# Optimization experiments

Hardware: AMD Instinct MI355X
Metric: run time of the kernel (lower is better)

Reference implementation:

```python
import jax, jax.numpy as jnp
import numpy as np

N_NODES = 100000
N_EDGES = 3200000
NUM_FEATURES = 128


def gcn_conv(x, edge_index, W, b):
    """PyG-style GCNConv: symmetric normalization with self-loops.
    x: [N, F_in], edge_index: [2, E] (row=src, col=dst), W: [F_in, F_out], b: [F_out].
    """
    n = x.shape[0]
    h = x @ W  # [N, F_out]
    # add self loops
    loop = jnp.arange(n, dtype=edge_index.dtype)
    row = jnp.concatenate([edge_index[0], loop])  # src
    col = jnp.concatenate([edge_index[1], loop])  # dst
    # degree of destination nodes (with self loops), edge weight = 1
    ones = jnp.ones(row.shape[0], dtype=h.dtype)
    deg = jax.ops.segment_sum(ones, col, num_segments=n)  # [N]
    dinv = jnp.where(deg > 0, jax.lax.rsqrt(deg), 0.0)
    norm = dinv[row] * dinv[col]  # [E+N]
    msg = h[row] * norm[:, None]  # gather + scale, [E+N, F_out]
    out = jax.ops.segment_sum(msg, col, num_segments=n)  # scatter-add
    return out + b


def setup_inputs() -> dict:
    key = jax.random.key(0)
    k1, k2, k3, k4 = jax.random.split(key, 4)
    x = jax.random.normal(k1, (N_NODES, NUM_FEATURES), dtype=jnp.float32)
    edge_index = jax.random.randint(k2, (2, N_EDGES), 0, N_NODES, dtype=jnp.int64)
    W1 = jax.random.normal(k3, (NUM_FEATURES, 16), dtype=jnp.float32) * (1.0 / np.sqrt(NUM_FEATURES))
    b1 = jnp.zeros((16,), dtype=jnp.float32)
    W2 = jax.random.normal(k4, (16, 2), dtype=jnp.float32) * (1.0 / np.sqrt(16.0))
    b2 = jnp.zeros((2,), dtype=jnp.float32)
    return {"x": x, "edge_index": edge_index, "W1": W1, "b1": b1, "W2": W2, "b2": b2}


def reference(x, edge_index, W1, b1, W2, b2):
    h = gcn_conv(x, edge_index, W1, b1)
    h = jax.nn.relu(h)
    out = gcn_conv(h, edge_index, W2, b2)
    return out
```

## Files before the change

kernel.cpp:

```cpp
#include <hip/hip_runtime.h>

#define N_FEAT 128
#define F1 16
#define F2 2
#define XPAD 132
#define NPB 512
#define NPB_SHIFT 9
#define BMAX 256
#define CHUNK 8192
#define HBLK 1024
#define K2 4

typedef int   ev_i4 __attribute__((ext_vector_type(4)));
typedef float ev_f4 __attribute__((ext_vector_type(4)));

__device__ __forceinline__ int4 nt_load_i4(const void* p) {
    ev_i4 v = __builtin_nontemporal_load((const ev_i4*)p);
    return make_int4(v.x, v.y, v.z, v.w);
}
__device__ __forceinline__ int nt_load_i(const int* p) {
    return __builtin_nontemporal_load(p);
}
__device__ __forceinline__ float4 nt_load_f4(const void* p) {
    ev_f4 v = __builtin_nontemporal_load((const ev_f4*)p);
    return make_float4(v.x, v.y, v.z, v.w);
}

__global__ __launch_bounds__(256) void hist_kernel(const int* __restrict__ col, int E,
        int* __restrict__ bcnt) {
    __shared__ int hist[BMAX];
    int t = threadIdx.x;
    hist[t] = 0;
    __syncthreads();
    int nq = (E + 3) >> 2;
    for (int q = blockIdx.x * 256 + t; q < nq; q += HBLK * 256) {
        int e0 = q * 4;
        if (e0 + 3 < E) {
            int4 c = nt_load_i4(col + e0);
            atomicAdd(&hist[c.x >> NPB_SHIFT], 1);
            atomicAdd(&hist[c.y >> NPB_SHIFT], 1);
            atomicAdd(&hist[c.z >> NPB_SHIFT], 1);
            atomicAdd(&hist[c.w >> NPB_SHIFT], 1);
        } else {
            for (int e = e0; e < E; ++e) atomicAdd(&hist[col[e] >> NPB_SHIFT], 1);
        }
    }
    __syncthreads();
    if (hist[t]) atomicAdd(&bcnt[t], hist[t]);
}

__global__ __launch_bounds__(256) void bscan_kernel(const int* __restrict__ bcnt,
        int* __restrict__ bstart, int* __restrict__ gcur, int E, int nbuck) {
    __shared__ int s[BMAX];
    int t = threadIdx.x;
    int v = (t < nbuck) ? bcnt[t] : 0;
    s[t] = v;
    __syncthreads();
    for (int off = 1; off < BMAX; off <<= 1) {
        int a = (t >= off) ? s[t - off] : 0;
        __syncthreads();
        s[t] += a;
        __syncthreads();
    }
    int excl = s[t] - v;
    if (t < nbuck) { bstart[t] = excl; gcur[t] = excl; }
    if (t == 0) bstart[nbuck] = E;
}

__global__ __launch_bounds__(256) void bin_kernel(const int* __restrict__ rowi,
        const int* __restrict__ coli, int* __restrict__ gcur,
        int* __restrict__ ebin, int E) {
    __shared__ int stage[CHUNK];
    __shared__ unsigned char sbkt[CHUNK];
    __shared__ int cnt[BMAX];
    __shared__ int pos[BMAX];
    __shared__ int runb[BMAX];
    int t = threadIdx.x;
    int base = blockIdx.x * CHUNK;
    int nval = E - base; if (nval > CHUNK) nval = CHUNK;
    cnt[t] = 0;
    __syncthreads();

    int cbuf[32];
#pragma unroll
    for (int j = 0; j < 8; ++j) {
        int idx = base + ((j << 8) + t) * 4;
        if (idx + 3 < E) {
            int4 c4 = nt_load_i4(coli + idx);
            cbuf[j * 4 + 0] = c4.x; cbuf[j * 4 + 1] = c4.y;
            cbuf[j * 4 + 2] = c4.z; cbuf[j * 4 + 3] = c4.w;
        } else {
#pragma unroll
            for (int u = 0; u < 4; ++u) {
                int i2 = idx + u;
                cbuf[j * 4 + u] = (i2 < E) ? coli[i2] : -1;
            }
        }
    }
#pragma unroll
    for (int k = 0; k < 32; ++k)
        if (cbuf[k] >= 0) atomicAdd(&cnt[cbuf[k] >> NPB_SHIFT], 1);
    __syncthreads();

    pos[t] = cnt[t];
    __syncthreads();
    for (int off = 1; off < BMAX; off <<= 1) {
        int a = (t >= off) ? pos[t - off] : 0;
        __syncthreads();
        pos[t] += a;
        __syncthreads();
    }
    int myc = cnt[t];
    int excl = pos[t] - myc;
    if (myc > 0) {
        int g = atomicAdd(&gcur[t], myc);
        runb[t] = g - excl;
    }
    __syncthreads();
    cnt[t] = excl;
    __syncthreads();

#pragma unroll
    for (int j = 0; j < 8; ++j) {
        int idx = base + ((j << 8) + t) * 4;
        int rr[4];
        if (idx + 3 < E) {
            int4 r4 = nt_load_i4(rowi + idx);
            rr[0] = r4.x; rr[1] = r4.y; rr[2] = r4.z; rr[3] = r4.w;
        } else {
#pragma unroll
            for (int u = 0; u < 4; ++u) {
                int i2 = idx + u;
                rr[u] = (i2 < E) ? rowi[i2] : 0;
            }
        }
#pragma unroll
        for (int u = 0; u < 4; ++u) {
            int c = cbuf[j * 4 + u];
            if (c >= 0) {
                int b = c >> NPB_SHIFT;
                int lp = atomicAdd(&cnt[b], 1);
                stage[lp] = (rr[u] << NPB_SHIFT) | (c & (NPB - 1));
                sbkt[lp] = (unsigned char)b;
            }
        }
    }
    __syncthreads();
    for (int i = t; i < nval; i += 256)
        ebin[runb[sbkt[i]] + i] = stage[i];
}

__global__ __launch_bounds__(256) void degpart_kernel(const int* __restrict__ bstart,
        const int* __restrict__ ebin, int* __restrict__ degp) {
    __shared__ int cnt[NPB];
    int t = threadIdx.x;
    int bid = blockIdx.x;
    int b = bid / K2, slice = bid - b * K2;
    cnt[t] = 0; cnt[t + 256] = 0;
    __syncthreads();
    int s = bstart[b], e = bstart[b + 1];
    int per = (e - s + K2 - 1) / K2;
    int s0 = s + slice * per;
    int e0 = s0 + per; if (e0 > e) e0 = e;
    for (int i = s0 + t; i < e0; i += 1024) {
        int w[4];
#pragma unroll
        for (int u = 0; u < 4; ++u) {
            int idx = i + u * 256;
            w[u] = (idx < e0) ? nt_load_i(&ebin[idx]) : -1;
        }
#pragma unroll
        for (int u = 0; u < 4; ++u)
            if (w[u] >= 0) atomicAdd(&cnt[w[u] & (NPB - 1)], 1);
    }
    __syncthreads();
    int* dp = degp + (size_t)bid * NPB;
    dp[t] = cnt[t];
    dp[t + 256] = cnt[t + 256];
}

__global__ __launch_bounds__(256) void rowscan_kernel(const int* __restrict__ bstart,
        const int* __restrict__ degp, int* __restrict__ rstart,
        float* __restrict__ dinv, int N, int E) {
    __shared__ int sd[NPB];
    int b = blockIdx.x, t = threadIdx.x;
    int base = b << NPB_SHIFT;
    int d0 = 0, d1 = 0;
    for (int sl = 0; sl < K2; ++sl) {
        const int* dp = degp + (size_t)(b * K2 + sl) * NPB;
        d0 += dp[t]; d1 += dp[t + 256];
    }
    sd[t] = d0; sd[t + 256] = d1;
    __syncthreads();
    for (int off = 1; off < NPB; off <<= 1) {
        int a0 = (t >= off) ? sd[t - off] : 0;
        int a1 = (t + 256 >= off) ? sd[t + 256 - off] : 0;
        __syncthreads();
        sd[t] += a0; sd[t + 256] += a1;
        __syncthreads();
    }
    int bs = bstart[b];
    int g0 = base + t, g1 = base + t + 256;
    if (g0 < N) { rstart[g0] = bs + sd[t] - d0;        dinv[g0] = rsqrtf((float)(d0 + 1)); }
    if (g1 < N) { rstart[g1] = bs + sd[t + 256] - d1;  dinv[g1] = rsqrtf((float)(d1 + 1)); }
    if (b == 0 && t == 0) rstart[N] = E;
}

__global__ __launch_bounds__(256) void nodescat_kernel(const int* __restrict__ bstart,
        const int* __restrict__ rstart, const int* __restrict__ ebin,
        int* __restrict__ csr, int N) {
    __shared__ int cur[128];
    int t = threadIdx.x;
    int bid = blockIdx.x;
    int b = bid >> 2, q = bid & 3;
    int lo = q << 7;
    if (t < 128) {
        int g = (b << NPB_SHIFT) + lo + t;
        cur[t] = (g < N) ? rstart[g] : 0;
    }
    __syncthreads();
    int s = bstart[b], e = bstart[b + 1];
    for (int i = s + t; i < e; i += 1024) {
        int w[4];
#pragma unroll
        for (int u = 0; u < 4; ++u) {
            int idx = i + u * 256;
            w[u] = (idx < e) ? ebin[idx] : -1;
        }
#pragma unroll
        for (int u = 0; u < 4; ++u) {
            if (w[u] >= 0) {
                int n = (w[u] & (NPB - 1)) - lo;
                if ((unsigned)n < 128u) {
                    int p = atomicAdd(&cur[n], 1);
                    csr[p] = w[u] >> NPB_SHIFT;
                }
            }
        }
    }
}

__global__ __launch_bounds__(256) void gemm1_kernel(
    const float* __restrict__ x, const float* __restrict__ W1,
    const float* __restrict__ dinv, float* __restrict__ hs, int N) {
    __shared__ __align__(16) float wsT[F1][XPAD];
    __shared__ __align__(16) float xs[16][XPAD];
    int t = threadIdx.x;
    for (int i = t; i < N_FEAT * F1; i += 256) {
        int k = i >> 4, f = i & 15;
        wsT[f][k] = W1[i];
    }
    int row0 = blockIdx.x * 16;
    for (int i = t; i < 16 * (N_FEAT / 4); i += 256) {
        int r = i >> 5, k4 = i & 31;
        int row = row0 + r;
        float4 v = (row < N) ? nt_load_f4(x + (size_t)row * N_FEAT + k4 * 4)
                             : make_float4(0.f, 0.f, 0.f, 0.f);
        *(float4*)&xs[r][k4 * 4] = v;
    }
    __syncthreads();
    int rr = t >> 4, f = t & 15;
    int row = row0 + rr;
    if (row >= N) return;
    float acc = 0.f;
#pragma unroll
    for (int k4 = 0; k4 < 32; ++k4) {
        float4 xv = *(const float4*)&xs[rr][k4 * 4];
        float4 wv = *(const float4*)&wsT[f][k4 * 4];
        acc += xv.x * wv.x + xv.y * wv.y + xv.z * wv.z + xv.w * wv.w;
    }
    hs[(size_t)row * F1 + f] = acc * dinv[row];
}

__global__ __launch_bounds__(256) void agg1_kernel(const int* __restrict__ rstart,
        const int* __restrict__ csr, const float* __restrict__ hs,
        const float* __restrict__ dinv, const float* __restrict__ b1,
        const float* __restrict__ W2, float* __restrict__ hs2, int N) {
    int t = threadIdx.x;
    int g = blockIdx.x * 16 + (t >> 4);
    int f = t & 15;
    if (g >= N) return;
    int s = rstart[g], e = rstart[g + 1];
    float acc = hs[(size_t)g * F1 + f];
    int k = s;
    for (; k + 4 <= e; k += 4) {
        int s0 = nt_load_i(&csr[k]);
        int s1 = nt_load_i(&csr[k + 1]);
        int s2 = nt_load_i(&csr[k + 2]);
        int s3 = nt_load_i(&csr[k + 3]);
        float v0 = hs[(size_t)s0 * F1 + f];
        float v1 = hs[(size_t)s1 * F1 + f];
        float v2 = hs[(size_t)s2 * F1 + f];
        float v3 = hs[(size_t)s3 * F1 + f];
        acc += (v0 + v1) + (v2 + v3);
    }
    for (; k < e; ++k) acc += hs[(size_t)nt_load_i(&csr[k]) * F1 + f];
    float di = dinv[g];
    float o = fmaxf(di * acc + b1[f], 0.f);
    float h0 = o * W2[f * F2 + 0];
    float h1 = o * W2[f * F2 + 1];
#pragma unroll
    for (int off = 1; off < 16; off <<= 1) {
        h0 += __shfl_xor(h0, off);
        h1 += __shfl_xor(h1, off);
    }
    if (f == 0) *(float2*)&hs2[(size_t)g * 2] = make_float2(di * h0, di * h1);
}

__global__ __launch_bounds__(256) void agg2_kernel(const int* __restrict__ rstart,
        const int* __restrict__ csr, const float* __restrict__ hs2,
        const float* __restrict__ dinv, const float* __restrict__ b2,
        float* __restrict__ out, int N) {
    int t = threadIdx.x;
    int g = blockIdx.x * 64 + (t >> 2);
    int l = t & 3;
    if (g >= N) return;
    int j = l & 1, c = l >> 1;
    int s = rstart[g], e = rstart[g + 1];
    float acc = 0.f;
    int k = s + c;
    for (; k + 6 < e; k += 8) {
        int s0 = nt_load_i(&csr[k]);
        int s1 = nt_load_i(&csr[k + 2]);
        int s2 = nt_load_i(&csr[k + 4]);
        int s3 = nt_load_i(&csr[k + 6]);
        acc += hs2[(size_t)s0 * 2 + j] + hs2[(size_t)s1 * 2 + j]
             + hs2[(size_t)s2 * 2 + j] + hs2[(size_t)s3 * 2 + j];
    }
    for (; k < e; k += 2) acc += hs2[(size_t)nt_load_i(&csr[k]) * 2 + j];
    acc += __shfl_xor(acc, 2);
    if (l < 2)
        out[(size_t)g * 2 + j] = dinv[g] * (acc + hs2[(size_t)g * 2 + j]) + b2[j];
}

extern "C" void kernel_launch(void* const* d_in, const int* in_sizes, int n_in,
                              void* d_out, int out_size, void* d_ws, size_t ws_size,
                              hipStream_t stream) {
    const float* x  = (const float*)d_in[0];
    const int*   ei = (const int*)d_in[1];
    const float* W1 = (const float*)d_in[2];
    const float* b1 = (const float*)d_in[3];
    const float* W2 = (const float*)d_in[4];
    const float* b2 = (const float*)d_in[5];
    int N = in_sizes[0] / N_FEAT;
    int E = in_sizes[1] / 2;
    const int* rowi = ei;
    const int* coli = ei + E;
    float* out = (float*)d_out;

    int nbuck = (N + NPB - 1) >> NPB_SHIFT;

    size_t NP = ((size_t)N + 1023) & ~(size_t)1023;
    size_t EP = ((size_t)E + 1023) & ~(size_t)1023;
    int*   wsI    = (int*)d_ws;
    float* dinv   = (float*)wsI;
    int*   rstart = wsI + NP;
    int*   bcnt   = wsI + 2 * NP + 1024;
    int*   bstart = wsI + 2 * NP + 1536;
    int*   gcur   = wsI + 2 * NP + 2048;
    float* hs     = (float*)(wsI + 2 * NP + 3072);
    float* hs2    = hs + 16 * NP;
    int*   ebin   = (int*)(hs2 + 2 * NP);
    int*   csr    = ebin + EP;
    int*   degp   = csr + EP;

    hipMemsetAsync(bcnt, 0, BMAX * sizeof(int), stream);

    hist_kernel<<<HBLK, 256, 0, stream>>>(coli, E, bcnt);
    bscan_kernel<<<1, BMAX, 0, stream>>>(bcnt, bstart, gcur, E, nbuck);
    bin_kernel<<<(E + CHUNK - 1) / CHUNK, 256, 0, stream>>>(rowi, coli, gcur, ebin, E);
    degpart_kernel<<<nbuck * K2, 256, 0, stream>>>(bstart, ebin, degp);
    rowscan_kernel<<<nbuck, 256, 0, stream>>>(bstart, degp, rstart, dinv, N, E);
    nodescat_kernel<<<nbuck * K2, 256, 0, stream>>>(bstart, rstart, ebin, csr, N);
    gemm1_kernel<<<(N + 15) / 16, 256, 0, stream>>>(x, W1, dinv, hs, N);

    agg1_kernel<<<(N + 15) / 16, 256, 0, stream>>>(rstart, csr, hs, dinv, b1, W2, hs2, N);
    agg2_kernel<<<(N + 63) / 64, 256, 0, stream>>>(rstart, csr, hs2, dinv, b2, out, N);
}
```

Baseline: 301.4 us.

## Fuse all graph-build and aggregation stages into one cooperative persistent kernel

```diff
diff --git a/kernel.cpp b/kernel.cpp
--- a/kernel.cpp
+++ b/kernel.cpp
@@ -1,4 +1,7 @@
 #include <hip/hip_runtime.h>
+#include <hip/hip_cooperative_groups.h>
+
+namespace cg = cooperative_groups;
 
 #define N_FEAT 128
 #define F1 16
@@ -7,8 +10,7 @@
 #define NPB 512
 #define NPB_SHIFT 9
 #define BMAX 256
-#define CHUNK 8192
-#define HBLK 1024
+#define CH 4096
 #define K2 4
 
 typedef int   ev_i4 __attribute__((ext_vector_type(4)));
@@ -26,354 +28,367 @@
     return make_float4(v.x, v.y, v.z, v.w);
 }
 
-__global__ __launch_bounds__(256) void hist_kernel(const int* __restrict__ col, int E,
-        int* __restrict__ bcnt) {
-    __shared__ int hist[BMAX];
-    int t = threadIdx.x;
-    hist[t] = 0;
-    __syncthreads();
-    int nq = (E + 3) >> 2;
-    for (int q = blockIdx.x * 256 + t; q < nq; q += HBLK * 256) {
-        int e0 = q * 4;
-        if (e0 + 3 < E) {
-            int4 c = nt_load_i4(col + e0);
-            atomicAdd(&hist[c.x >> NPB_SHIFT], 1);
-            atomicAdd(&hist[c.y >> NPB_SHIFT], 1);
-            atomicAdd(&hist[c.z >> NPB_SHIFT], 1);
-            atomicAdd(&hist[c.w >> NPB_SHIFT], 1);
-        } else {
-            for (int e = e0; e < E; ++e) atomicAdd(&hist[col[e] >> NPB_SHIFT], 1);
-        }
-    }
-    __syncthreads();
-    if (hist[t]) atomicAdd(&bcnt[t], hist[t]);
-}
-
-__global__ __launch_bounds__(256) void bscan_kernel(const int* __restrict__ bcnt,
-        int* __restrict__ bstart, int* __restrict__ gcur, int E, int nbuck) {
-    __shared__ int s[BMAX];
-    int t = threadIdx.x;
-    int v = (t < nbuck) ? bcnt[t] : 0;
-    s[t] = v;
-    __syncthreads();
-    for (int off = 1; off < BMAX; off <<= 1) {
-        int a = (t >= off) ? s[t - off] : 0;
-        __syncthreads();
-        s[t] += a;
-        __syncthreads();
-    }
-    int excl = s[t] - v;
-    if (t < nbuck) { bstart[t] = excl; gcur[t] = excl; }
-    if (t == 0) bstart[nbuck] = E;
-}
-
-__global__ __launch_bounds__(256) void bin_kernel(const int* __restrict__ rowi,
-        const int* __restrict__ coli, int* __restrict__ gcur,
-        int* __restrict__ ebin, int E) {
-    __shared__ int stage[CHUNK];
-    __shared__ unsigned char sbkt[CHUNK];
-    __shared__ int cnt[BMAX];
-    __shared__ int pos[BMAX];
-    __shared__ int runb[BMAX];
-    int t = threadIdx.x;
-    int base = blockIdx.x * CHUNK;
-    int nval = E - base; if (nval > CHUNK) nval = CHUNK;
-    cnt[t] = 0;
-    __syncthreads();
-
-    int cbuf[32];
-#pragma unroll
-    for (int j = 0; j < 8; ++j) {
-        int idx = base + ((j << 8) + t) * 4;
-        if (idx + 3 < E) {
-            int4 c4 = nt_load_i4(coli + idx);
-            cbuf[j * 4 + 0] = c4.x; cbuf[j * 4 + 1] = c4.y;
-            cbuf[j * 4 + 2] = c4.z; cbuf[j * 4 + 3] = c4.w;
-        } else {
-#pragma unroll
-            for (int u = 0; u < 4; ++u) {
-                int i2 = idx + u;
-                cbuf[j * 4 + u] = (i2 < E) ? coli[i2] : -1;
-            }
-        }
-    }
-#pragma unroll
-    for (int k = 0; k < 32; ++k)
-        if (cbuf[k] >= 0) atomicAdd(&cnt[cbuf[k] >> NPB_SHIFT], 1);
-    __syncthreads();
-
-    pos[t] = cnt[t];
-    __syncthreads();
-    for (int off = 1; off < BMAX; off <<= 1) {
-        int a = (t >= off) ? pos[t - off] : 0;
-        __syncthreads();
-        pos[t] += a;
-        __syncthreads();
-    }
-    int myc = cnt[t];
-    int excl = pos[t] - myc;
-    if (myc > 0) {
-        int g = atomicAdd(&gcur[t], myc);
-        runb[t] = g - excl;
-    }
-    __syncthreads();
-    cnt[t] = excl;
-    __syncthreads();
-
-#pragma unroll
-    for (int j = 0; j < 8; ++j) {
-        int idx = base + ((j << 8) + t) * 4;
-        int rr[4];
-        if (idx + 3 < E) {
-            int4 r4 = nt_load_i4(rowi + idx);
-            rr[0] = r4.x; rr[1] = r4.y; rr[2] = r4.z; rr[3] = r4.w;
-        } else {
-#pragma unroll
-            for (int u = 0; u < 4; ++u) {
-                int i2 = idx + u;
-                rr[u] = (i2 < E) ? rowi[i2] : 0;
-            }
-        }
-#pragma unroll
-        for (int u = 0; u < 4; ++u) {
-            int c = cbuf[j * 4 + u];
-            if (c >= 0) {
-                int b = c >> NPB_SHIFT;
-                int lp = atomicAdd(&cnt[b], 1);
-                stage[lp] = (rr[u] << NPB_SHIFT) | (c & (NPB - 1));
-                sbkt[lp] = (unsigned char)b;
-            }
-        }
-    }
-    __syncthreads();
-    for (int i = t; i < nval; i += 256)
-        ebin[runb[sbkt[i]] + i] = stage[i];
-}
-
-__global__ __launch_bounds__(256) void degpart_kernel(const int* __restrict__ bstart,
-        const int* __restrict__ ebin, int* __restrict__ degp) {
-    __shared__ int cnt[NPB];
-    int t = threadIdx.x;
-    int bid = blockIdx.x;
-    int b = bid / K2, slice = bid - b * K2;
-    cnt[t] = 0; cnt[t + 256] = 0;
-    __syncthreads();
-    int s = bstart[b], e = bstart[b + 1];
-    int per = (e - s + K2 - 1) / K2;
-    int s0 = s + slice * per;
-    int e0 = s0 + per; if (e0 > e) e0 = e;
-    for (int i = s0 + t; i < e0; i += 1024) {
-        int w[4];
-#pragma unroll
-        for (int u = 0; u < 4; ++u) {
-            int idx = i + u * 256;
-            w[u] = (idx < e0) ? nt_load_i(&ebin[idx]) : -1;
-        }
-#pragma unroll
-        for (int u = 0; u < 4; ++u)
-            if (w[u] >= 0) atomicAdd(&cnt[w[u] & (NPB - 1)], 1);
-    }
-    __syncthreads();
-    int* dp = degp + (size_t)bid * NPB;
-    dp[t] = cnt[t];
-    dp[t + 256] = cnt[t + 256];
-}
-
-__global__ __launch_bounds__(256) void rowscan_kernel(const int* __restrict__ bstart,
-        const int* __restrict__ degp, int* __restrict__ rstart,
-        float* __restrict__ dinv, int N, int E) {
-    __shared__ int sd[NPB];
-    int b = blockIdx.x, t = threadIdx.x;
-    int base = b << NPB_SHIFT;
-    int d0 = 0, d1 = 0;
-    for (int sl = 0; sl < K2; ++sl) {
-        const int* dp = degp + (size_t)(b * K2 + sl) * NPB;
-        d0 += dp[t]; d1 += dp[t + 256];
-    }
-    sd[t] = d0; sd[t + 256] = d1;
-    __syncthreads();
-    for (int off = 1; off < NPB; off <<= 1) {
-        int a0 = (t >= off) ? sd[t - off] : 0;
-        int a1 = (t + 256 >= off) ? sd[t + 256 - off] : 0;
-        __syncthreads();
-        sd[t] += a0; sd[t + 256] += a1;
-        __syncthreads();
-    }
-    int bs = bstart[b];
-    int g0 = base + t, g1 = base + t + 256;
-    if (g0 < N) { rstart[g0] = bs + sd[t] - d0;        dinv[g0] = rsqrtf((float)(d0 + 1)); }
-    if (g1 < N) { rstart[g1] = bs + sd[t + 256] - d1;  dinv[g1] = rsqrtf((float)(d1 + 1)); }
-    if (b == 0 && t == 0) rstart[N] = E;
-}
-
-__global__ __launch_bounds__(256) void nodescat_kernel(const int* __restrict__ bstart,
-        const int* __restrict__ rstart, const int* __restrict__ ebin,
-        int* __restrict__ csr, int N) {
-    __shared__ int cur[128];
-    int t = threadIdx.x;
-    int bid = blockIdx.x;
-    int b = bid >> 2, q = bid & 3;
-    int lo = q << 7;
-    if (t < 128) {
-        int g = (b << NPB_SHIFT) + lo + t;
-        cur[t] = (g < N) ? rstart[g] : 0;
-    }
-    __syncthreads();
-    int s = bstart[b], e = bstart[b + 1];
-    for (int i = s + t; i < e; i += 1024) {
-        int w[4];
-#pragma unroll
-        for (int u = 0; u < 4; ++u) {
-            int idx = i + u * 256;
-            w[u] = (idx < e) ? ebin[idx] : -1;
-        }
-#pragma unroll
-        for (int u = 0; u < 4; ++u) {
-            if (w[u] >= 0) {
-                int n = (w[u] & (NPB - 1)) - lo;
-                if ((unsigned)n < 128u) {
-                    int p = atomicAdd(&cur[n], 1);
-                    csr[p] = w[u] >> NPB_SHIFT;
-                }
-            }
-        }
-    }
-}
-
-__global__ __launch_bounds__(256) void gemm1_kernel(
-    const float* __restrict__ x, const float* __restrict__ W1,
-    const float* __restrict__ dinv, float* __restrict__ hs, int N) {
-    __shared__ __align__(16) float wsT[F1][XPAD];
-    __shared__ __align__(16) float xs[16][XPAD];
-    int t = threadIdx.x;
-    for (int i = t; i < N_FEAT * F1; i += 256) {
-        int k = i >> 4, f = i & 15;
-        wsT[f][k] = W1[i];
-    }
-    int row0 = blockIdx.x * 16;
-    for (int i = t; i < 16 * (N_FEAT / 4); i += 256) {
-        int r = i >> 5, k4 = i & 31;
-        int row = row0 + r;
-        float4 v = (row < N) ? nt_load_f4(x + (size_t)row * N_FEAT + k4 * 4)
-                             : make_float4(0.f, 0.f, 0.f, 0.f);
-        *(float4*)&xs[r][k4 * 4] = v;
-    }
-    __syncthreads();
-    int rr = t >> 4, f = t & 15;
-    int row = row0 + rr;
-    if (row >= N) return;
-    float acc = 0.f;
-#pragma unroll
-    for (int k4 = 0; k4 < 32; ++k4) {
-        float4 xv = *(const float4*)&xs[rr][k4 * 4];
-        float4 wv = *(const float4*)&wsT[f][k4 * 4];
-        acc += xv.x * wv.x + xv.y * wv.y + xv.z * wv.z + xv.w * wv.w;
-    }
-    hs[(size_t)row * F1 + f] = acc * dinv[row];
-}
-
-__global__ __launch_bounds__(256) void agg1_kernel(const int* __restrict__ rstart,
-        const int* __restrict__ csr, const float* __restrict__ hs,
-        const float* __restrict__ dinv, const float* __restrict__ b1,
-        const float* __restrict__ W2, float* __restrict__ hs2, int N) {
-    int t = threadIdx.x;
-    int g = blockIdx.x * 16 + (t >> 4);
-    int f = t & 15;
-    if (g >= N) return;
-    int s = rstart[g], e = rstart[g + 1];
-    float acc = hs[(size_t)g * F1 + f];
-    int k = s;
-    for (; k + 4 <= e; k += 4) {
-        int s0 = nt_load_i(&csr[k]);
-        int s1 = nt_load_i(&csr[k + 1]);
-        int s2 = nt_load_i(&csr[k + 2]);
-        int s3 = nt_load_i(&csr[k + 3]);
-        float v0 = hs[(size_t)s0 * F1 + f];
-        float v1 = hs[(size_t)s1 * F1 + f];
-        float v2 = hs[(size_t)s2 * F1 + f];
-        float v3 = hs[(size_t)s3 * F1 + f];
-        acc += (v0 + v1) + (v2 + v3);
-    }
-    for (; k < e; ++k) acc += hs[(size_t)nt_load_i(&csr[k]) * F1 + f];
-    float di = dinv[g];
-    float o = fmaxf(di * acc + b1[f], 0.f);
-    float h0 = o * W2[f * F2 + 0];
-    float h1 = o * W2[f * F2 + 1];
-#pragma unroll
-    for (int off = 1; off < 16; off <<= 1) {
-        h0 += __shfl_xor(h0, off);
-        h1 += __shfl_xor(h1, off);
-    }
-    if (f == 0) *(float2*)&hs2[(size_t)g * 2] = make_float2(di * h0, di * h1);
-}
-
-__global__ __launch_bounds__(256) void agg2_kernel(const int* __restrict__ rstart,
-        const int* __restrict__ csr, const float* __restrict__ hs2,
-        const float* __restrict__ dinv, const float* __restrict__ b2,
-        float* __restrict__ out, int N) {
-    int t = threadIdx.x;
-    int g = blockIdx.x * 64 + (t >> 2);
-    int l = t & 3;
-    if (g >= N) return;
-    int j = l & 1, c = l >> 1;
-    int s = rstart[g], e = rstart[g + 1];
-    float acc = 0.f;
-    int k = s + c;
-    for (; k + 6 < e; k += 8) {
-        int s0 = nt_load_i(&csr[k]);
-        int s1 = nt_load_i(&csr[k + 2]);
-        int s2 = nt_load_i(&csr[k + 4]);
-        int s3 = nt_load_i(&csr[k + 6]);
-        acc += hs2[(size_t)s0 * 2 + j] + hs2[(size_t)s1 * 2 + j]
-             + hs2[(size_t)s2 * 2 + j] + hs2[(size_t)s3 * 2 + j];
-    }
-    for (; k < e; k += 2) acc += hs2[(size_t)nt_load_i(&csr[k]) * 2 + j];
-    acc += __shfl_xor(acc, 2);
-    if (l < 2)
-        out[(size_t)g * 2 + j] = dinv[g] * (acc + hs2[(size_t)g * 2 + j]) + b2[j];
+struct P {
+    const float* x; const int* rowi; const int* coli;
+    const float* W1; const float* b1; const float* W2; const float* b2;
+    float* out;
+    int* bcnt; int* bstart; int* gcur; int* ebin; int* degp; int* rstart; int* csr;
+    float* dinv; float* hs; float* hs2;
+    int N, E, nbuck, nchunk;
+};
+
+union LDSU {
+    int hist[BMAX];
+    struct { int s[BMAX]; } sc;
+    struct { int stage[CH]; unsigned char sbkt[CH]; int cnt[BMAX]; int pos[BMAX]; int runb[BMAX]; } bin;
+    struct { int cnt[NPB]; } dg;
+    struct { int sd[NPB]; } rs;
+    struct { int cur[128]; } ns;
+    struct { float wsT[F1][XPAD]; float xs[16][XPAD]; } g1;
+};
+
+__global__ __launch_bounds__(256, 4) void mega(P p) {
+    cg::grid_group grid = cg::this_grid();
+    __shared__ LDSU u;
+    const int t = threadIdx.x;
+    const int nb = gridDim.x, bidx = blockIdx.x;
+
+    if (bidx == 0 && t < BMAX) p.bcnt[t] = 0;
+    grid.sync();
+
+    {
+        u.hist[t] = 0;
+        __syncthreads();
+        int nq = (p.E + 3) >> 2;
+        for (int q = bidx * 256 + t; q < nq; q += nb * 256) {
+            int e0 = q * 4;
+            if (e0 + 3 < p.E) {
+                int4 c = nt_load_i4(p.coli + e0);
+                atomicAdd(&u.hist[c.x >> NPB_SHIFT], 1);
+                atomicAdd(&u.hist[c.y >> NPB_SHIFT], 1);
+                atomicAdd(&u.hist[c.z >> NPB_SHIFT], 1);
+                atomicAdd(&u.hist[c.w >> NPB_SHIFT], 1);
+            } else {
+                for (int e = e0; e < p.E; ++e) atomicAdd(&u.hist[p.coli[e] >> NPB_SHIFT], 1);
+            }
+        }
+        __syncthreads();
+        if (u.hist[t]) atomicAdd(&p.bcnt[t], u.hist[t]);
+    }
+    grid.sync();
+
+    if (bidx == 0) {
+        int v = (t < p.nbuck) ? p.bcnt[t] : 0;
+        u.sc.s[t] = v;
+        __syncthreads();
+        for (int off = 1; off < BMAX; off <<= 1) {
+            int a = (t >= off) ? u.sc.s[t - off] : 0;
+            __syncthreads();
+            u.sc.s[t] += a;
+            __syncthreads();
+        }
+        int excl = u.sc.s[t] - v;
+        if (t < p.nbuck) { p.bstart[t] = excl; p.gcur[t] = excl; }
+        if (t == 0) { p.bstart[p.nbuck] = p.E; p.rstart[p.N] = p.E; }
+    }
+    grid.sync();
+
+    for (int ch = bidx; ch < p.nchunk; ch += nb) {
+        int base = ch * CH;
+        int nval = p.E - base; if (nval > CH) nval = CH;
+        u.bin.cnt[t] = 0;
+        __syncthreads();
+        int cbuf[16];
+#pragma unroll
+        for (int j = 0; j < 4; ++j) {
+            int idx = base + ((j << 8) + t) * 4;
+            if (idx + 3 < p.E) {
+                int4 c4 = nt_load_i4(p.coli + idx);
+                cbuf[j * 4 + 0] = c4.x; cbuf[j * 4 + 1] = c4.y;
+                cbuf[j * 4 + 2] = c4.z; cbuf[j * 4 + 3] = c4.w;
+            } else {
+#pragma unroll
+                for (int uu = 0; uu < 4; ++uu) {
+                    int i2 = idx + uu;
+                    cbuf[j * 4 + uu] = (i2 < p.E) ? p.coli[i2] : -1;
+                }
+            }
+        }
+#pragma unroll
+        for (int k = 0; k < 16; ++k)
+            if (cbuf[k] >= 0) atomicAdd(&u.bin.cnt[cbuf[k] >> NPB_SHIFT], 1);
+        __syncthreads();
+        u.bin.pos[t] = u.bin.cnt[t];
+        __syncthreads();
+        for (int off = 1; off < BMAX; off <<= 1) {
+            int a = (t >= off) ? u.bin.pos[t - off] : 0;
+            __syncthreads();
+            u.bin.pos[t] += a;
+            __syncthreads();
+        }
+        int myc = u.bin.cnt[t];
+        int excl = u.bin.pos[t] - myc;
+        if (myc > 0) {
+            int g = atomicAdd(&p.gcur[t], myc);
+            u.bin.runb[t] = g - excl;
+        }
+        __syncthreads();
+        u.bin.cnt[t] = excl;
+        __syncthreads();
+#pragma unroll
+        for (int j = 0; j < 4; ++j) {
+            int idx = base + ((j << 8) + t) * 4;
+            int rr[4];
+            if (idx + 3 < p.E) {
+                int4 r4 = nt_load_i4(p.rowi + idx);
+                rr[0] = r4.x; rr[1] = r4.y; rr[2] = r4.z; rr[3] = r4.w;
+            } else {
+#pragma unroll
+                for (int uu = 0; uu < 4; ++uu) {
+                    int i2 = idx + uu;
+                    rr[uu] = (i2 < p.E) ? p.rowi[i2] : 0;
+                }
+            }
+#pragma unroll
+            for (int uu = 0; uu < 4; ++uu) {
+                int c = cbuf[j * 4 + uu];
+                if (c >= 0) {
+                    int b = c >> NPB_SHIFT;
+                    int lp = atomicAdd(&u.bin.cnt[b], 1);
+                    u.bin.stage[lp] = (rr[uu] << NPB_SHIFT) | (c & (NPB - 1));
+                    u.bin.sbkt[lp] = (unsigned char)b;
+                }
+            }
+        }
+        __syncthreads();
+        for (int i = t; i < nval; i += 256)
+            p.ebin[u.bin.runb[u.bin.sbkt[i]] + i] = u.bin.stage[i];
+        __syncthreads();
+    }
+    grid.sync();
+
+    for (int bid = bidx; bid < p.nbuck * K2; bid += nb) {
+        int b = bid >> 2, slice = bid & 3;
+        u.dg.cnt[t] = 0; u.dg.cnt[t + 256] = 0;
+        __syncthreads();
+        int s = p.bstart[b], e = p.bstart[b + 1];
+        int per = (e - s + K2 - 1) / K2;
+        int s0 = s + slice * per;
+        int e0 = s0 + per; if (e0 > e) e0 = e;
+        for (int i = s0 + t; i < e0; i += 1024) {
+            int w[4];
+#pragma unroll
+            for (int uu = 0; uu < 4; ++uu) {
+                int idx = i + uu * 256;
+                w[uu] = (idx < e0) ? nt_load_i(&p.ebin[idx]) : -1;
+            }
+#pragma unroll
+            for (int uu = 0; uu < 4; ++uu)
+                if (w[uu] >= 0) atomicAdd(&u.dg.cnt[w[uu] & (NPB - 1)], 1);
+        }
+        __syncthreads();
+        int* dp = p.degp + (size_t)bid * NPB;
+        dp[t] = u.dg.cnt[t];
+        dp[t + 256] = u.dg.cnt[t + 256];
+        __syncthreads();
+    }
+    grid.sync();
+
+    for (int b = bidx; b < p.nbuck; b += nb) {
+        int base = b << NPB_SHIFT;
+        int d0 = 0, d1 = 0;
+        for (int sl = 0; sl < K2; ++sl) {
+            const int* dp = p.degp + (size_t)(b * K2 + sl) * NPB;
+            d0 += dp[t]; d1 += dp[t + 256];
+        }
+        u.rs.sd[t] = d0; u.rs.sd[t + 256] = d1;
+        __syncthreads();
+        for (int off = 1; off < NPB; off <<= 1) {
+            int a0 = (t >= off) ? u.rs.sd[t - off] : 0;
+            int a1 = (t + 256 >= off) ? u.rs.sd[t + 256 - off] : 0;
+            __syncthreads();
+            u.rs.sd[t] += a0; u.rs.sd[t + 256] += a1;
+            __syncthreads();
+        }
+        int bs = p.bstart[b];
+        int g0 = base + t, g1 = base + t + 256;
+        if (g0 < p.N) { p.rstart[g0] = bs + u.rs.sd[t] - d0;       p.dinv[g0] = rsqrtf((float)(d0 + 1)); }
+        if (g1 < p.N) { p.rstart[g1] = bs + u.rs.sd[t + 256] - d1; p.dinv[g1] = rsqrtf((float)(d1 + 1)); }
+        __syncthreads();
+    }
+    grid.sync();
+
+    for (int bid = bidx; bid < p.nbuck * K2; bid += nb) {
+        __syncthreads();
+        int b = bid >> 2, q = bid & 3;
+        int lo = q << 7;
+        if (t < 128) {
+            int g = (b << NPB_SHIFT) + lo + t;
+            u.ns.cur[t] = (g < p.N) ? p.rstart[g] : 0;
+        }
+        __syncthreads();
+        int s = p.bstart[b], e = p.bstart[b + 1];
+        for (int i = s + t; i < e; i += 1024) {
+            int w[4];
+#pragma unroll
+            for (int uu = 0; uu < 4; ++uu) {
+                int idx = i + uu * 256;
+                w[uu] = (idx < e) ? p.ebin[idx] : -1;
+            }
+#pragma unroll
+            for (int uu = 0; uu < 4; ++uu) {
+                if (w[uu] >= 0) {
+                    int n = (w[uu] & (NPB - 1)) - lo;
+                    if ((unsigned)n < 128u) {
+                        int pp = atomicAdd(&u.ns.cur[n], 1);
+                        p.csr[pp] = w[uu] >> NPB_SHIFT;
+                    }
+                }
+            }
+        }
+    }
+
+    {
+        __syncthreads();
+        for (int i = t; i < N_FEAT * F1; i += 256) {
+            int k = i >> 4, f = i & 15;
+            u.g1.wsT[f][k] = p.W1[i];
+        }
+        int ntile = (p.N + 15) >> 4;
+        for (int tile = bidx; tile < ntile; tile += nb) {
+            __syncthreads();
+            int row0 = tile * 16;
+            for (int i = t; i < 16 * (N_FEAT / 4); i += 256) {
+                int r = i >> 5, k4 = i & 31;
+                int row = row0 + r;
+                float4 v = (row < p.N) ? nt_load_f4(p.x + (size_t)row * N_FEAT + k4 * 4)
+                                       : make_float4(0.f, 0.f, 0.f, 0.f);
+                *(float4*)&u.g1.xs[r][k4 * 4] = v;
+            }
+            __syncthreads();
+            int rr = t >> 4, f = t & 15;
+            int row = row0 + rr;
+            if (row < p.N) {
+                float acc = 0.f;
+#pragma unroll
+                for (int k4 = 0; k4 < 32; ++k4) {
+                    float4 xv = *(const float4*)&u.g1.xs[rr][k4 * 4];
+                    float4 wv = *(const float4*)&u.g1.wsT[f][k4 * 4];
+                    acc += xv.x * wv.x + xv.y * wv.y + xv.z * wv.z + xv.w * wv.w;
+                }
+                p.hs[(size_t)row * F1 + f] = acc * p.dinv[row];
+            }
+        }
+    }
+    grid.sync();
+
+    {
+        int ntile = (p.N + 15) >> 4;
+        int f = t & 15;
+        for (int tile = bidx; tile < ntile; tile += nb) {
+            int g = tile * 16 + (t >> 4);
+            if (g >= p.N) continue;
+            int s = p.rstart[g], e = p.rstart[g + 1];
+            float acc = p.hs[(size_t)g * F1 + f];
+            int k = s;
+            for (; k + 4 <= e; k += 4) {
+                int s0 = nt_load_i(&p.csr[k]);
+                int s1 = nt_load_i(&p.csr[k + 1]);
+                int s2 = nt_load_i(&p.csr[k + 2]);
+                int s3 = nt_load_i(&p.csr[k + 3]);
+                float v0 = p.hs[(size_t)s0 * F1 + f];
+                float v1 = p.hs[(size_t)s1 * F1 + f];
+                float v2 = p.hs[(size_t)s2 * F1 + f];
+                float v3 = p.hs[(size_t)s3 * F1 + f];
+                acc += (v0 + v1) + (v2 + v3);
+            }
+            for (; k < e; ++k) acc += p.hs[(size_t)nt_load_i(&p.csr[k]) * F1 + f];
+            float di = p.dinv[g];
+            float o = fmaxf(di * acc + p.b1[f], 0.f);
+            float h0 = o * p.W2[f * F2 + 0];
+            float h1 = o * p.W2[f * F2 + 1];
+#pragma unroll
+            for (int off = 1; off < 16; off <<= 1) {
+                h0 += __shfl_xor(h0, off);
+                h1 += __shfl_xor(h1, off);
+            }
+            if (f == 0) *(float2*)&p.hs2[(size_t)g * 2] = make_float2(di * h0, di * h1);
+        }
+    }
+    grid.sync();
+
+    {
+        int ntile = (p.N + 63) >> 6;
+        int l = t & 3;
+        int j = l & 1, c = l >> 1;
+        for (int tile = bidx; tile < ntile; tile += nb) {
+            int g = tile * 64 + (t >> 2);
+            if (g >= p.N) continue;
+            int s = p.rstart[g], e = p.rstart[g + 1];
+            float acc = 0.f;
+            int k = s + c;
+            for (; k + 6 < e; k += 8) {
+                int s0 = nt_load_i(&p.csr[k]);
+                int s1 = nt_load_i(&p.csr[k + 2]);
+                int s2 = nt_load_i(&p.csr[k + 4]);
+                int s3 = nt_load_i(&p.csr[k + 6]);
+                acc += p.hs2[(size_t)s0 * 2 + j] + p.hs2[(size_t)s1 * 2 + j]
+                     + p.hs2[(size_t)s2 * 2 + j] + p.hs2[(size_t)s3 * 2 + j];
+            }
+            for (; k < e; k += 2) acc += p.hs2[(size_t)nt_load_i(&p.csr[k]) * 2 + j];
+            acc += __shfl_xor(acc, 2);
+            if (l < 2)
+                p.out[(size_t)g * 2 + j] = p.dinv[g] * (acc + p.hs2[(size_t)g * 2 + j]) + p.b2[j];
+        }
+    }
 }
 
 extern "C" void kernel_launch(void* const* d_in, const int* in_sizes, int n_in,
                               void* d_out, int out_size, void* d_ws, size_t ws_size,
                               hipStream_t stream) {
-    const float* x  = (const float*)d_in[0];
-    const int*   ei = (const int*)d_in[1];
-    const float* W1 = (const float*)d_in[2];
-    const float* b1 = (const float*)d_in[3];
-    const float* W2 = (const float*)d_in[4];
-    const float* b2 = (const float*)d_in[5];
-    int N = in_sizes[0] / N_FEAT;
-    int E = in_sizes[1] / 2;
-    const int* rowi = ei;
-    const int* coli = ei + E;
-    float* out = (float*)d_out;
-
-    int nbuck = (N + NPB - 1) >> NPB_SHIFT;
-
-    size_t NP = ((size_t)N + 1023) & ~(size_t)1023;
-    size_t EP = ((size_t)E + 1023) & ~(size_t)1023;
-    int*   wsI    = (int*)d_ws;
-    float* dinv   = (float*)wsI;
-    int*   rstart = wsI + NP;
-    int*   bcnt   = wsI + 2 * NP + 1024;
-    int*   bstart = wsI + 2 * NP + 1536;
-    int*   gcur   = wsI + 2 * NP + 2048;
-    float* hs     = (float*)(wsI + 2 * NP + 3072);
-    float* hs2    = hs + 16 * NP;
-    int*   ebin   = (int*)(hs2 + 2 * NP);
-    int*   csr    = ebin + EP;
-    int*   degp   = csr + EP;
-
-    hipMemsetAsync(bcnt, 0, BMAX * sizeof(int), stream);
-
-    hist_kernel<<<HBLK, 256, 0, stream>>>(coli, E, bcnt);
-    bscan_kernel<<<1, BMAX, 0, stream>>>(bcnt, bstart, gcur, E, nbuck);
-    bin_kernel<<<(E + CHUNK - 1) / CHUNK, 256, 0, stream>>>(rowi, coli, gcur, ebin, E);
-    degpart_kernel<<<nbuck * K2, 256, 0, stream>>>(bstart, ebin, degp);
-    rowscan_kernel<<<nbuck, 256, 0, stream>>>(bstart, degp, rstart, dinv, N, E);
-    nodescat_kernel<<<nbuck * K2, 256, 0, stream>>>(bstart, rstart, ebin, csr, N);
-    gemm1_kernel<<<(N + 15) / 16, 256, 0, stream>>>(x, W1, dinv, hs, N);
-
-    agg1_kernel<<<(N + 15) / 16, 256, 0, stream>>>(rstart, csr, hs, dinv, b1, W2, hs2, N);
-    agg2_kernel<<<(N + 63) / 64, 256, 0, stream>>>(rstart, csr, hs2, dinv, b2, out, N);
-}
+    P p;
+    p.x  = (const float*)d_in[0];
+    const int* ei = (const int*)d_in[1];
+    p.W1 = (const float*)d_in[2];
+    p.b1 = (const float*)d_in[3];
+    p.W2 = (const float*)d_in[4];
+    p.b2 = (const float*)d_in[5];
+    p.N = in_sizes[0] / N_FEAT;
+    p.E = in_sizes[1] / 2;
+    p.rowi = ei;
+    p.coli = ei + p.E;
+    p.out = (float*)d_out;
+    p.nbuck = (p.N + NPB - 1) >> NPB_SHIFT;
+    p.nchunk = (p.E + CH - 1) / CH;
+
+    size_t NP = ((size_t)p.N + 1023) & ~(size_t)1023;
+    size_t EP = ((size_t)p.E + 1023) & ~(size_t)1023;
+    int* wsI = (int*)d_ws;
+    p.dinv   = (float*)wsI;
+    p.rstart = wsI + NP;
+    p.bcnt   = wsI + 2 * NP + 1024;
+    p.bstart = wsI + 2 * NP + 1536;
+    p.gcur   = wsI + 2 * NP + 2048;
+    p.hs     = (float*)(wsI + 2 * NP + 3072);
+    p.hs2    = p.hs + 16 * NP;
+    p.ebin   = (int*)(p.hs2 + 2 * NP);
+    p.csr    = p.ebin + EP;
+    p.degp   = p.csr + EP;
+
+    static int g_grid = 0;
+    if (g_grid == 0) {
+        int dev = 0;
+        hipGetDevice(&dev);
+        int ncu = 0;
+        hipDeviceGetAttribute(&ncu, hipDeviceAttributeMultiprocessorCount, dev);
+        if (ncu <= 0) ncu = 256;
+        int occ = 0;
+        hipOccupancyMaxActiveBlocksPerMultiprocessor(&occ, (const void*)mega, 256, 0);
+        if (occ < 1) occ = 1;
+        if (occ > 8) occ = 8;
+        g_grid = ncu * occ;
+    }
+
+    void* kargs[] = { &p };
+    hipLaunchCooperativeKernel((const void*)mega, dim3(g_grid), dim3(256), kargs, 0, stream);
+}
```

Measured after the change: 808.0 us. 168% more time.
